# Optimization experiments

Hardware: AMD Instinct MI355X
Metric: run time of the kernel (lower is better)

## Reference

```python
import jax, jax.numpy as jnp
import numpy as np

HEADS = 8

def _conv1x1(x, W, b):
    # x: [n, Cin, H, W]; W: [Cout, Cin]; b: [Cout]
    return jnp.einsum('nchw,oc->nohw', x, W) + b[None, :, None, None]

def setup_inputs() -> dict:
    key = jax.random.key(0)
    ks = jax.random.split(key, 11)
    n, Cin, H, W = 8, 256, 80, 80
    Ck, Cv = 256, 256
    s_in = 1.0 / np.sqrt(Cin)
    s_v = 1.0 / np.sqrt(Cv)
    return {
        'query_feature': jax.random.normal(ks[0], (n, Cin, H, W), jnp.float32),
        'key_feature': jax.random.normal(ks[1], (n, Cin, H, W), jnp.float32),
        'value_feature': jax.random.normal(ks[2], (n, Cin, H, W), jnp.float32),
        'Wq': jax.random.normal(ks[3], (Ck, Cin), jnp.float32) * s_in,
        'bq': jax.random.normal(ks[4], (Ck,), jnp.float32) * s_in,
        'Wk': jax.random.normal(ks[5], (Ck, Cin), jnp.float32) * s_in,
        'bk': jax.random.normal(ks[6], (Ck,), jnp.float32) * s_in,
        'Wv': jax.random.normal(ks[7], (Cv, Cin), jnp.float32) * s_in,
        'bv': jax.random.normal(ks[8], (Cv,), jnp.float32) * s_in,
        'Wr': jax.random.normal(ks[9], (Cin, Cv), jnp.float32) * s_v,
        'br': jax.random.normal(ks[10], (Cin,), jnp.float32) * s_v,
    }

def reference(query_feature, key_feature, value_feature, Wq, bq, Wk, bk, Wv, bv, Wr, br):
    n, _, qh, qw = query_feature.shape
    kvn, _, kvh, kvw = key_feature.shape
    Ck = Wq.shape[0]
    Cv = Wv.shape[0]
    hk = Ck // HEADS
    hv = Cv // HEADS
    Lq = qh * qw
    Lkv = kvh * kvw
    # 1x1 conv projections, split channels into heads (consecutive channel blocks)
    q = _conv1x1(query_feature, Wq, bq).reshape(n, HEADS, hk, Lq)
    k = _conv1x1(key_feature, Wk, bk).reshape(kvn, HEADS, hk, Lkv)
    v = _conv1x1(value_feature, Wv, bv).reshape(kvn, HEADS, hv, Lkv)
    # softmax: keys over spatial positions, queries over head channels
    k = jax.nn.softmax(k, axis=3)
    q = jax.nn.softmax(q, axis=2)
    # efficient (linear) attention: context = K @ V^T, out = context^T @ Q
    context = jnp.einsum('nhkl,nhvl->nhkv', k, v)          # [n, H, hk, hv]
    attended = jnp.einsum('nhkv,nhkl->nhvl', context, q)   # [n, H, hv, Lq]
    aggregated = attended.reshape(n, Cv, qh, qw)
    return _conv1x1(aggregated, Wr, br) + query_feature
```

## Files before the change

### kernel.cpp

```cpp
#include <hip/hip_runtime.h>
#include <hip/hip_bf16.h>

#define NB 8
#define C 256
#define LL 6400
#define HEADS 8
#define HC 32
#define NH 64
#define SEG 40
#define SL 160
#define QPP 264

typedef unsigned short u16;
typedef unsigned int u32;
typedef __attribute__((ext_vector_type(8))) short bf16x8;
typedef __attribute__((ext_vector_type(4))) float f32x4;

typedef __attribute__((address_space(1))) const u32 ga_u32;
typedef __attribute__((address_space(3))) u32 ls_u32;

__device__ __forceinline__ void gload_lds16(const u16* g, u16* l) {
  __builtin_amdgcn_global_load_lds((ga_u32*)g, (ls_u32*)l, 16, 0, 0);
}

__device__ __forceinline__ float bf2f(u32 u) { return __uint_as_float(u << 16); }
__device__ __forceinline__ u16 f2bf(float f) {
  __hip_bfloat16 h = __float2bfloat16(f);
  return *(u16*)&h;
}
__device__ __forceinline__ void unpack8(uint4 u, float* f) {
  f[0] = bf2f(u.x & 0xffffu); f[1] = bf2f(u.x >> 16);
  f[2] = bf2f(u.y & 0xffffu); f[3] = bf2f(u.y >> 16);
  f[4] = bf2f(u.z & 0xffffu); f[5] = bf2f(u.z >> 16);
  f[6] = bf2f(u.w & 0xffffu); f[7] = bf2f(u.w >> 16);
}

struct WcvtArgs { const float* W[3]; u16* Wb[3]; };
struct XcvtArgs { const float* X[3]; u16* Xb[3]; };
struct PFArgs { const u16* Xb[3]; const u16* Wb[3]; const float* bias[3]; u16* P[3]; };

__global__ __launch_bounds__(256) void wcvt(WcvtArgs a) {
  const int idx = blockIdx.x * 256 + threadIdx.x;
  const int which = idx >> 13, r = idx & 8191;
  const int co = r >> 5, c8 = r & 31;
  const float* src = a.W[which] + co * 256 + c8 * 8;
  float4 v0 = *(const float4*)src, v1 = *(const float4*)(src + 4);
  union { bf16x8 v; u16 h[8]; } o;
  o.h[0] = f2bf(v0.x); o.h[1] = f2bf(v0.y); o.h[2] = f2bf(v0.z); o.h[3] = f2bf(v0.w);
  o.h[4] = f2bf(v1.x); o.h[5] = f2bf(v1.y); o.h[6] = f2bf(v1.z); o.h[7] = f2bf(v1.w);
  const int p = (c8 & ~3) | ((c8 & 3) ^ ((co >> 1) & 3));
  *(bf16x8*)&a.Wb[which][co * 256 + p * 8] = o.v;
}

__global__ __launch_bounds__(256) void xcvt(XcvtArgs a) {
  __shared__ float tile[64][68];
  const int l0 = blockIdx.x * 64;
  const int ct = blockIdx.y;
  const int pz = blockIdx.z;
  const int which = pz >> 3, n = pz & 7;
  const int t = threadIdx.x;
  const float* X = a.X[which] + (size_t)n * C * LL;
  const int cr = t >> 2, lq = t & 3;
#pragma unroll
  for (int p = 0; p < 4; ++p) {
    float4 v = *(const float4*)&X[(size_t)(ct * 64 + cr) * LL + l0 + (lq * 4 + p) * 4];
    *(float4*)&tile[cr][(lq * 4 + p) * 4] = v;
  }
  __syncthreads();
  u16* Xb = a.Xb[which] + (size_t)n * LL * C;
  const int u3 = t & 7;
#pragma unroll
  for (int w2 = 0; w2 < 2; ++w2) {
    const int lc = (t >> 3) + w2 * 32;
    union { bf16x8 v; u16 h[8]; } o;
#pragma unroll
    for (int e = 0; e < 8; ++e) {
      const int ep = e ^ u3;
      o.h[ep] = f2bf(tile[u3 * 8 + ep][lc]);
    }
    const int p3 = u3 ^ (lc & 7);
    *(bf16x8*)&Xb[(size_t)(l0 + lc) * C + (ct * 8 + p3) * 8] = o.v;
  }
}

__global__ __launch_bounds__(256, 2) void proj_fused(PFArgs args) {
  __shared__ __align__(16) u16 Xp[64 * 256];
  __shared__ __align__(16) u16 Bs[2][256 * 32];
  const int which = blockIdx.y >> 3, n = blockIdx.y & 7;
  const int l0 = blockIdx.x * 64;
  const int t = threadIdx.x;
  const int lane = t & 63, wave = t >> 6;
  const int fr = lane & 15, q = lane >> 4;
  const int wl = (wave & 1) * 32, wco = (wave >> 1) * 128;
  const int srow = t >> 2, scol = (t & 3) * 8;
  const u16* Xb = args.Xb[which] + (size_t)n * LL * C;
  const u16* Wb = args.Wb[which];

#pragma unroll
  for (int s = 0; s < 8; ++s) {
    const int rp = wave * 8 + s;
    gload_lds16(&Xb[(size_t)(l0 + rp * 2) * C + lane * 8], &Xp[rp * 512]);
  }
#pragma unroll
  for (int s = 0; s < 4; ++s)
    gload_lds16(&Wb[(size_t)(s * 64 + srow) * C + scol], &Bs[0][s * 2048 + wave * 512]);
  __syncthreads();

  f32x4 acc[2][8] = {};
  const int sco = (fr >> 1) & 3;
#pragma unroll
  for (int kt = 0; kt < 8; ++kt) {
    if (kt < 7) {
#pragma unroll
      for (int s = 0; s < 4; ++s)
        gload_lds16(&Wb[(size_t)(s * 64 + srow) * C + (kt + 1) * 32 + scol],
                    &Bs[(kt + 1) & 1][s * 2048 + wave * 512]);
    }
    bf16x8 a[2];
#pragma unroll
    for (int i = 0; i < 2; ++i) {
      const int row = wl + i * 16 + fr;
      a[i] = *(const bf16x8*)&Xp[row * 256 + (((kt * 4 + q) ^ (row & 7)) * 8)];
    }
#pragma unroll
    for (int j = 0; j < 8; ++j) {
      bf16x8 b = *(const bf16x8*)&Bs[kt & 1][(wco + j * 16 + fr) * 32 + ((q ^ sco) * 8)];
#pragma unroll
      for (int i = 0; i < 2; ++i)
        acc[i][j] = __builtin_amdgcn_mfma_f32_16x16x32_bf16(a[i], b, acc[i][j], 0, 0, 0);
    }
    __syncthreads();
  }

  const float* bias = args.bias[which];
  u16* P = args.P[which] + (size_t)n * LL * C;
  float bb[8];
#pragma unroll
  for (int j = 0; j < 8; ++j) bb[j] = bias[wco + j * 16 + fr];
#pragma unroll
  for (int i = 0; i < 2; ++i)
#pragma unroll
    for (int r = 0; r < 4; ++r) {
      const int lrow = wl + i * 16 + q * 4 + r;
#pragma unroll
      for (int j = 0; j < 8; ++j)
        Xp[lrow * 256 + wco + j * 16 + fr] = f2bf(acc[i][j][r] + bb[j]);
    }
  __syncthreads();
  const int rg = t >> 5, ch = t & 31;
#pragma unroll
  for (int s = 0; s < 8; ++s) {
    const int row = rg * 8 + s;
    bf16x8 vrow = *(const bf16x8*)&Xp[row * 256 + ch * 8];
    *(bf16x8*)&P[(size_t)(l0 + row) * C + ch * 8] = vrow;
  }
}

__global__ __launch_bounds__(256) void ctx_part(const u16* __restrict__ Kt,
    const u16* __restrict__ Vt, float* __restrict__ pctx, float* __restrict__ psum) {
  __shared__ __align__(16) u16 Ks[16 * 256];
  __shared__ __align__(16) u16 Vs[16 * 256];
  const int seg = blockIdx.x, n = blockIdx.y;
  const int t = threadIdx.x, lane = t & 63, wave = t >> 6;
  const int l0 = seg * SL;
  const u16* KtN = Kt + (size_t)n * LL * C;
  const u16* VtN = Vt + (size_t)n * LL * C;
  const int k4 = (lane & 7) * 4, v8 = lane >> 3;
  float acc[2][4][4] = {};
  float ssum[2][4] = {};
  for (int ls = 0; ls < SL; ls += 16) {
    __syncthreads();
#pragma unroll
    for (int i = 0; i < 2; ++i) {
      const int r = wave * 4 + i * 2;
      gload_lds16(&KtN[(size_t)(l0 + ls + r) * C + lane * 8], &Ks[r * 256]);
      gload_lds16(&VtN[(size_t)(l0 + ls + r) * C + lane * 8], &Vs[r * 256]);
    }
    __syncthreads();
#pragma unroll
    for (int hh = 0; hh < 2; ++hh) {
      const int h = wave * 2 + hh;
#pragma unroll
      for (int l = 0; l < 16; ++l) {
        ushort4 ku = *(const ushort4*)&Ks[l * 256 + h * 32 + k4];
        ushort4 vu = *(const ushort4*)&Vs[l * 256 + h * 32 + v8 * 4];
        float ek[4] = {__expf(bf2f(ku.x)), __expf(bf2f(ku.y)),
                       __expf(bf2f(ku.z)), __expf(bf2f(ku.w))};
        float vf[4] = {bf2f(vu.x), bf2f(vu.y), bf2f(vu.z), bf2f(vu.w)};
#pragma unroll
        for (int i = 0; i < 4; ++i)
#pragma unroll
          for (int j = 0; j < 4; ++j) acc[hh][i][j] = fmaf(ek[i], vf[j], acc[hh][i][j]);
        if (v8 == 0)
#pragma unroll
          for (int i = 0; i < 4; ++i) ssum[hh][i] += ek[i];
      }
    }
  }
#pragma unroll
  for (int hh = 0; hh < 2; ++hh) {
    const int h = wave * 2 + hh;
    const size_t pb = ((size_t)seg * NH + n * 8 + h) * 1024;
#pragma unroll
    for (int i = 0; i < 4; ++i)
#pragma unroll
      for (int j = 0; j < 4; ++j)
        pctx[pb + (size_t)(k4 + i) * 32 + v8 * 4 + j] = acc[hh][i][j];
    if (v8 == 0) {
      const size_t sb = ((size_t)seg * NH + n * 8 + h) * 32;
#pragma unroll
      for (int i = 0; i < 4; ++i) psum[sb + k4 + i] = ssum[hh][i];
    }
  }
}

__global__ __launch_bounds__(256) void ctx_reduce(const float* __restrict__ pctx,
    const float* __restrict__ psum, float* __restrict__ ctx) {
  const int idx = blockIdx.x * 256 + threadIdx.x;
  const int nh = idx >> 10, e = idx & 1023, k = e >> 5;
  float s = 0.f, ss = 0.f;
  for (int g = 0; g < SEG; ++g) {
    s += pctx[(size_t)(g * NH + nh) * 1024 + e];
    ss += psum[(size_t)(g * NH + nh) * 32 + k];
  }
  ctx[idx] = s / ss;
}

__global__ __launch_bounds__(256) void mfuse(const float* __restrict__ Wr,
    const float* __restrict__ ctx, u16* __restrict__ M) {
  const int idx = blockIdx.x * 256 + threadIdx.x;
  const int hk = idx & 255;
  const int o = (idx >> 8) & 255;
  const int n = idx >> 16;
  const int h = hk >> 5, k = hk & 31;
  const float* wr = Wr + (size_t)o * C + h * HC;
  const float* cx = ctx + ((size_t)(n * HEADS + h) * HC + k) * HC;
  float s = 0.f;
#pragma unroll
  for (int v = 0; v < HC; ++v) s = fmaf(wr[v], cx[v], s);
  M[idx] = f2bf(s);
}

__global__ __launch_bounds__(256) void out_fused(const u16* __restrict__ Qt,
    const u16* __restrict__ Mb, const float* __restrict__ br,
    const float* __restrict__ Xq, float* __restrict__ out) {
  __shared__ __align__(16) u16 Qp[64 * QPP];
  __shared__ __align__(16) u16 As[2][128 * 32];
  const int n = blockIdx.y, l0 = blockIdx.x * 64;
  const int t = threadIdx.x, lane = t & 63, wave = t >> 6;
  const int fr = lane & 15, q = lane >> 4;
  const int wcoL = (wave >> 1) * 64, wl = (wave & 1) * 32;
  const int srow = t >> 2, scol = (t & 3) * 8;
  const u16* QtN = Qt + (size_t)n * LL * C;
  const u16* MbN = Mb + (size_t)n * C * C;

#pragma unroll
  for (int s = 0; s < 2; ++s)
    gload_lds16(&MbN[(size_t)(s * 64 + srow) * C + scol], &As[0][s * 2048 + wave * 512]);

#pragma unroll
  for (int p = 0; p < 2; ++p) {
    const int row = p * 32 + (t >> 3);
    const int g = t & 7;
    const uint4* src = (const uint4*)&QtN[(size_t)(l0 + row) * C + g * 32];
    uint4 u0 = src[0], u1 = src[1], u2 = src[2], u3 = src[3];
    float v[32];
    unpack8(u0, v); unpack8(u1, v + 8); unpack8(u2, v + 16); unpack8(u3, v + 24);
    float e[32], s = 0.f;
#pragma unroll
    for (int j = 0; j < 32; ++j) { e[j] = __expf(v[j]); s += e[j]; }
    const float r = 1.0f / s;
    uint4* drow = (uint4*)&Qp[row * QPP + g * 32];
#pragma unroll
    for (int b4 = 0; b4 < 4; ++b4) {
      union { uint4 u; u16 h[8]; } o;
#pragma unroll
      for (int j = 0; j < 8; ++j) o.h[j] = f2bf(e[b4 * 8 + j] * r);
      drow[b4] = o.u;
    }
  }
  asm volatile("s_waitcnt vmcnt(0) lgkmcnt(0)" ::: "memory");
  __builtin_amdgcn_s_barrier();
  __builtin_amdgcn_sched_barrier(0);

  f32x4 acc[2][4][2] = {};
#pragma unroll
  for (int it = 0; it < 16; ++it) {
    const int coh = it >> 3, k0 = (it & 7) * 32, cur = it & 1;
    if (it < 15) {
      const int nco = (it + 1) >> 3, nk0 = ((it + 1) & 7) * 32;
#pragma unroll
      for (int s = 0; s < 2; ++s)
        gload_lds16(&MbN[(size_t)(nco * 128 + s * 64 + srow) * C + nk0 + scol],
                    &As[cur ^ 1][s * 2048 + wave * 512]);
      __builtin_amdgcn_sched_barrier(0);
    }
    bf16x8 a[4], b[2];
#pragma unroll
    for (int i = 0; i < 4; ++i)
      a[i] = *(const bf16x8*)&As[cur][(wcoL + i * 16 + fr) * 32 + q * 8];
#pragma unroll
    for (int j = 0; j < 2; ++j)
      b[j] = *(const bf16x8*)&Qp[(wl + j * 16 + fr) * QPP + k0 + q * 8];
#pragma unroll
    for (int i = 0; i < 4; ++i)
#pragma unroll
      for (int j = 0; j < 2; ++j)
        acc[coh][i][j] = __builtin_amdgcn_mfma_f32_16x16x32_bf16(a[i], b[j], acc[coh][i][j], 0, 0, 0);
    if (it < 15) {
      asm volatile("s_waitcnt vmcnt(0) lgkmcnt(0)" ::: "memory");
      __builtin_amdgcn_s_barrier();
      __builtin_amdgcn_sched_barrier(0);
    }
  }

  const float* XqN = Xq + (size_t)n * C * LL;
  float* On = out + (size_t)n * C * LL;
#pragma unroll
  for (int coh = 0; coh < 2; ++coh)
#pragma unroll
    for (int i = 0; i < 4; ++i)
#pragma unroll
      for (int r = 0; r < 4; ++r) {
        const int co = coh * 128 + wcoL + i * 16 + q * 4 + r;
        const float bb = br[co];
#pragma unroll
        for (int j = 0; j < 2; ++j) {
          const int l = l0 + wl + j * 16 + fr;
          const size_t off = (size_t)co * LL + l;
          On[off] = acc[coh][i][j][r] + bb + XqN[off];
        }
      }
}

extern "C" void kernel_launch(void* const* d_in, const int* in_sizes, int n_in,
                              void* d_out, int out_size, void* d_ws, size_t ws_size,
                              hipStream_t stream) {
  const float* Xq = (const float*)d_in[0];
  const float* Xk = (const float*)d_in[1];
  const float* Xv = (const float*)d_in[2];
  const float* Wq = (const float*)d_in[3];
  const float* bq = (const float*)d_in[4];
  const float* Wk = (const float*)d_in[5];
  const float* bk = (const float*)d_in[6];
  const float* Wv = (const float*)d_in[7];
  const float* bv = (const float*)d_in[8];
  const float* Wr = (const float*)d_in[9];
  const float* br = (const float*)d_in[10];
  float* out = (float*)d_out;

  char* ws = (char*)d_ws;
  const size_t nelem = (size_t)NB * LL * C;
  u16* Qt = (u16*)ws;
  u16* Kt = (u16*)(ws + nelem * 2);
  u16* Vt = (u16*)(ws + nelem * 4);
  char* p = ws + nelem * 6;
  u16* Wqb = (u16*)p; p += C * C * 2;
  u16* Wkb = (u16*)p; p += C * C * 2;
  u16* Wvb = (u16*)p; p += C * C * 2;
  float* pctx = (float*)p; p += (size_t)SEG * NH * HC * HC * 4;
  float* psum = (float*)p; p += (size_t)SEG * NH * HC * 4;
  float* ctx = (float*)p;  p += (size_t)NH * HC * HC * 4;
  u16* Mb = (u16*)p;

  WcvtArgs wa;
  wa.W[0] = Wq; wa.W[1] = Wk; wa.W[2] = Wv;
  wa.Wb[0] = Wqb; wa.Wb[1] = Wkb; wa.Wb[2] = Wvb;
  wcvt<<<96, 256, 0, stream>>>(wa);

  XcvtArgs xa;
  xa.X[0] = Xq; xa.X[1] = Xk; xa.X[2] = Xv;
  xa.Xb[0] = Qt; xa.Xb[1] = Kt; xa.Xb[2] = Vt;
  xcvt<<<dim3(100, 4, 24), 256, 0, stream>>>(xa);

  PFArgs pa;
  pa.Xb[0] = Qt; pa.Xb[1] = Kt; pa.Xb[2] = Vt;
  pa.Wb[0] = Wqb; pa.Wb[1] = Wkb; pa.Wb[2] = Wvb;
  pa.bias[0] = bq; pa.bias[1] = bk; pa.bias[2] = bv;
  pa.P[0] = Qt; pa.P[1] = Kt; pa.P[2] = Vt;
  proj_fused<<<dim3(100, 24), 256, 0, stream>>>(pa);

  ctx_part<<<dim3(SEG, NB), 256, 0, stream>>>(Kt, Vt, pctx, psum);
  ctx_reduce<<<NH * HC * HC / 256, 256, 0, stream>>>(pctx, psum, ctx);
  mfuse<<<NB * C * C / 256, 256, 0, stream>>>(Wr, ctx, Mb);
  out_fused<<<dim3(100, NB), 256, 0, stream>>>(Qt, Mb, br, Xq, out);
}
```

Before: 380.1 us.

## Fuse fp32-to-bf16 input transpose into projection GEMM kernel

```diff
diff --git a/kernel.cpp b/kernel.cpp
--- a/kernel.cpp
+++ b/kernel.cpp
@@ -36,8 +36,7 @@
 }
 
 struct WcvtArgs { const float* W[3]; u16* Wb[3]; };
-struct XcvtArgs { const float* X[3]; u16* Xb[3]; };
-struct PFArgs { const u16* Xb[3]; const u16* Wb[3]; const float* bias[3]; u16* P[3]; };
+struct PFArgs { const float* X[3]; const u16* Wb[3]; const float* bias[3]; u16* P[3]; };
 
 __global__ __launch_bounds__(256) void wcvt(WcvtArgs a) {
   const int idx = blockIdx.x * 256 + threadIdx.x;
@@ -52,39 +51,9 @@
   *(bf16x8*)&a.Wb[which][co * 256 + p * 8] = o.v;
 }
 
-__global__ __launch_bounds__(256) void xcvt(XcvtArgs a) {
-  __shared__ float tile[64][68];
-  const int l0 = blockIdx.x * 64;
-  const int ct = blockIdx.y;
-  const int pz = blockIdx.z;
-  const int which = pz >> 3, n = pz & 7;
-  const int t = threadIdx.x;
-  const float* X = a.X[which] + (size_t)n * C * LL;
-  const int cr = t >> 2, lq = t & 3;
-#pragma unroll
-  for (int p = 0; p < 4; ++p) {
-    float4 v = *(const float4*)&X[(size_t)(ct * 64 + cr) * LL + l0 + (lq * 4 + p) * 4];
-    *(float4*)&tile[cr][(lq * 4 + p) * 4] = v;
-  }
-  __syncthreads();
-  u16* Xb = a.Xb[which] + (size_t)n * LL * C;
-  const int u3 = t & 7;
-#pragma unroll
-  for (int w2 = 0; w2 < 2; ++w2) {
-    const int lc = (t >> 3) + w2 * 32;
-    union { bf16x8 v; u16 h[8]; } o;
-#pragma unroll
-    for (int e = 0; e < 8; ++e) {
-      const int ep = e ^ u3;
-      o.h[ep] = f2bf(tile[u3 * 8 + ep][lc]);
-    }
-    const int p3 = u3 ^ (lc & 7);
-    *(bf16x8*)&Xb[(size_t)(l0 + lc) * C + (ct * 8 + p3) * 8] = o.v;
-  }
-}
-
 __global__ __launch_bounds__(256, 2) void proj_fused(PFArgs args) {
-  __shared__ __align__(16) u16 Xp[64 * 256];
+  __shared__ __align__(16) float Xs[64 * 64];
+  __shared__ __align__(16) u16 Ap[64 * 256];
   __shared__ __align__(16) u16 Bs[2][256 * 32];
   const int which = blockIdx.y >> 3, n = blockIdx.y & 7;
   const int l0 = blockIdx.x * 64;
@@ -93,18 +62,37 @@
   const int fr = lane & 15, q = lane >> 4;
   const int wl = (wave & 1) * 32, wco = (wave >> 1) * 128;
   const int srow = t >> 2, scol = (t & 3) * 8;
-  const u16* Xb = args.Xb[which] + (size_t)n * LL * C;
+  const float* X = args.X[which] + (size_t)n * C * LL;
   const u16* Wb = args.Wb[which];
 
-#pragma unroll
-  for (int s = 0; s < 8; ++s) {
-    const int rp = wave * 8 + s;
-    gload_lds16(&Xb[(size_t)(l0 + rp * 2) * C + lane * 8], &Xp[rp * 512]);
-  }
 #pragma unroll
   for (int s = 0; s < 4; ++s)
     gload_lds16(&Wb[(size_t)(s * 64 + srow) * C + scol], &Bs[0][s * 2048 + wave * 512]);
-  __syncthreads();
+
+#pragma unroll
+  for (int qt = 0; qt < 4; ++qt) {
+#pragma unroll
+    for (int s = 0; s < 4; ++s) {
+      const int r = wave * 16 + s * 4;
+      gload_lds16((const u16*)&X[(size_t)(qt * 64 + r + (lane >> 4)) * LL + l0 + (lane & 15) * 4],
+                  (u16*)&Xs[r * 64]);
+    }
+    __syncthreads();
+#pragma unroll
+    for (int g = 0; g < 2; ++g) {
+      const int cg = wave * 2 + g;
+      float v[8];
+#pragma unroll
+      for (int e = 0; e < 8; ++e) v[e] = Xs[(cg * 8 + e) * 64 + lane];
+      union { uint4 u; u32 w[4]; } pk;
+#pragma unroll
+      for (int p = 0; p < 4; ++p)
+        pk.w[p] = (u32)f2bf(v[2 * p]) | ((u32)f2bf(v[2 * p + 1]) << 16);
+      const int cb = qt * 8 + cg;
+      *(uint4*)&Ap[lane * 256 + (cb ^ (lane & 7)) * 8] = pk.u;
+    }
+    __syncthreads();
+  }
 
   f32x4 acc[2][8] = {};
   const int sco = (fr >> 1) & 3;
@@ -120,7 +108,7 @@
 #pragma unroll
     for (int i = 0; i < 2; ++i) {
       const int row = wl + i * 16 + fr;
-      a[i] = *(const bf16x8*)&Xp[row * 256 + (((kt * 4 + q) ^ (row & 7)) * 8)];
+      a[i] = *(const bf16x8*)&Ap[row * 256 + (((kt * 4 + q) ^ (row & 7)) * 8)];
     }
 #pragma unroll
     for (int j = 0; j < 8; ++j) {
@@ -144,14 +132,14 @@
       const int lrow = wl + i * 16 + q * 4 + r;
 #pragma unroll
       for (int j = 0; j < 8; ++j)
-        Xp[lrow * 256 + wco + j * 16 + fr] = f2bf(acc[i][j][r] + bb[j]);
+        Ap[lrow * 256 + wco + j * 16 + fr] = f2bf(acc[i][j][r] + bb[j]);
     }
   __syncthreads();
   const int rg = t >> 5, ch = t & 31;
 #pragma unroll
   for (int s = 0; s < 8; ++s) {
     const int row = rg * 8 + s;
-    bf16x8 vrow = *(const bf16x8*)&Xp[row * 256 + ch * 8];
+    bf16x8 vrow = *(const bf16x8*)&Ap[row * 256 + ch * 8];
     *(bf16x8*)&P[(size_t)(l0 + row) * C + ch * 8] = vrow;
   }
 }
@@ -368,13 +356,8 @@
   wa.Wb[0] = Wqb; wa.Wb[1] = Wkb; wa.Wb[2] = Wvb;
   wcvt<<<96, 256, 0, stream>>>(wa);
 
-  XcvtArgs xa;
-  xa.X[0] = Xq; xa.X[1] = Xk; xa.X[2] = Xv;
-  xa.Xb[0] = Qt; xa.Xb[1] = Kt; xa.Xb[2] = Vt;
-  xcvt<<<dim3(100, 4, 24), 256, 0, stream>>>(xa);
-
   PFArgs pa;
-  pa.Xb[0] = Qt; pa.Xb[1] = Kt; pa.Xb[2] = Vt;
+  pa.X[0] = Xq; pa.X[1] = Xk; pa.X[2] = Xv;
   pa.Wb[0] = Wqb; pa.Wb[1] = Wkb; pa.Wb[2] = Wvb;
   pa.bias[0] = bq; pa.bias[1] = bk; pa.bias[2] = bv;
   pa.P[0] = Qt; pa.P[1] = Kt; pa.P[2] = Vt;
```

New measurement: 334.6 us. 12.0% less time.
